# Kernel optimization log

Hardware: AMD Instinct MI355X
Metric: run time of the kernel (lower is better)

## Reference

```python
import jax, jax.numpy as jnp
import numpy as np

N_HASHES = 4
CHUNK = 144
REDUCTION = 4

# PyTorch bicubic (a=-0.75), align_corners=False, integer scale 2 ->
# fixed fractional offsets t=0.75 (even outputs) and t=0.25 (odd outputs).
_EW = jnp.array([-0.03515625, 0.26171875, 0.87890625, -0.10546875], jnp.float32)
_OW = _EW[::-1]


def _up2_axis(x, axis):
    n = x.shape[axis]
    pad = [(0, 0)] * x.ndim
    pad[axis] = (2, 2)
    xp = jnp.pad(x, pad, mode='edge')  # torch clamps border indices
    sl = lambda s: jax.lax.slice_in_dim(xp, s, s + n, axis=axis)
    even = sum(_EW[k] * sl(k) for k in range(4))
    odd = sum(_OW[k] * sl(k + 1) for k in range(4))
    out = jnp.stack([even, odd], axis=axis + 1)
    shp = list(x.shape)
    shp[axis] = 2 * n
    return out.reshape(shp)


def bicubic_up2(x):
    return _up2_axis(_up2_axis(x, 2), 3)


def conv2d(x, w, b, pad):
    y = jax.lax.conv_general_dilated(x, w, (1, 1), [(pad, pad), (pad, pad)],
                                     dimension_numbers=('NCHW', 'OIHW', 'NCHW'))
    return y + b[None, :, None, None]


def _adj(t):
    # attend to own + two adjacent buckets along chunk axis (axis=2)
    return jnp.concatenate([t, jnp.roll(t, 1, axis=2), jnp.roll(t, -1, axis=2)], axis=3)


def nlsa(x, wm, bm, wa, ba, rot):
    N, Cc, H, W = x.shape
    L = H * W
    xe = conv2d(x, wm, bm, 1).reshape(N, -1, L).transpose(0, 2, 1)  # [N,L,C]
    ye = conv2d(x, wa, ba, 0).reshape(N, -1, L).transpose(0, 2, 1)  # [N,L,C*red]
    C = xe.shape[-1]
    hash_buckets = min(L // CHUNK + (L // CHUNK) % 2, 128)
    # LSH: random rotations -> argmax bucket codes (non-differentiable, detached)
    rotated = jnp.einsum('btf,fhi->bhti', xe, rot)  # [N,h,L,hb//2]
    rotated = jnp.concatenate([rotated, -rotated], axis=-1)  # [N,h,L,hb]
    codes = jnp.argmax(rotated, axis=-1)  # [N,h,L]
    codes = codes + (jnp.arange(N_HASHES) * hash_buckets)[None, :, None]
    codes = jax.lax.stop_gradient(codes.reshape(N, -1))  # [N,h*L]
    indices = jnp.argsort(codes, axis=-1)
    undo = jnp.argsort(indices, axis=-1)
    mod = indices % L
    xs = jnp.take_along_axis(xe, mod[..., None], axis=1)  # [N,h*L,C]
    ys = jnp.take_along_axis(ye, mod[..., None], axis=1)  # [N,h*L,C*red]
    padding = (-L) % CHUNK
    xb = xs.reshape(N, N_HASHES, L, C)
    yb = ys.reshape(N, N_HASHES, L, C * REDUCTION)
    if padding:
        xb = jnp.concatenate([xb, xb[:, :, -padding:, :]], axis=2)
        yb = jnp.concatenate([yb, yb[:, :, -padding:, :]], axis=2)
    nch = xb.shape[2] // CHUNK
    xb = xb.reshape(N, N_HASHES, nch, CHUNK, C)
    yb = yb.reshape(N, N_HASHES, nch, CHUNK, C * REDUCTION)
    xm = xb / jnp.maximum(jnp.linalg.norm(xb, axis=-1, keepdims=True), 5e-5)
    xm = _adj(xm)      # [N,h,k,3*chunk,C]
    ybj = _adj(yb)     # [N,h,k,3*chunk,C*red]
    raw = jnp.einsum('bhkie,bhkje->bhkij', xb, xm)  # [N,h,k,chunk,3*chunk]
    bscore = jax.scipy.special.logsumexp(raw, axis=-1, keepdims=True)
    score = jnp.exp(raw - bscore)
    ret = jnp.einsum('bhkij,bhkje->bhkie', score, ybj)
    ret = ret.reshape(N, N_HASHES, -1, C * REDUCTION)
    bscore = bscore.reshape(N, N_HASHES, -1)
    if padding:
        ret = ret[:, :, :-padding]
        bscore = bscore[:, :, :-padding]
    ret = ret.reshape(N, -1, C * REDUCTION)
    bscore = bscore.reshape(N, -1)
    ret = jnp.take_along_axis(ret, undo[..., None], axis=1)
    bscore = jnp.take_along_axis(bscore, undo, axis=1)
    ret = ret.reshape(N, N_HASHES, L, C * REDUCTION)
    probs = jax.nn.softmax(bscore.reshape(N, N_HASHES, L, 1), axis=1)
    ret = jnp.sum(ret * probs, axis=1)  # [N,L,C*red]
    return ret.transpose(0, 2, 1).reshape(N, -1, H, W) + x


def setup_inputs() -> dict:
    key = jax.random.key(0)
    ks = jax.random.split(key, 8)
    w = lambda k, shape, fan: (jax.random.normal(k, shape, jnp.float32) / np.sqrt(fan)).astype(jnp.float32)
    return {
        'x': jax.random.normal(ks[0], (2, 64, 96, 96), jnp.float32),
        'w1': w(ks[1], (64, 64, 3, 3), 64 * 9), 'b1': jnp.zeros((64,), jnp.float32),
        'w2': w(ks[2], (64, 64, 3, 3), 64 * 9), 'b2': jnp.zeros((64,), jnp.float32),
        'wm': w(ks[3], (16, 64, 3, 3), 64 * 9), 'bm': jnp.zeros((16,), jnp.float32),
        'wa': w(ks[4], (64, 64, 1, 1), 64), 'ba': jnp.zeros((64,), jnp.float32),
        'rot': jax.random.normal(ks[5], (16, N_HASHES, 64), jnp.float32),  # [C, h, hash_buckets//2]
    }


def reference(x, w1, b1, w2, b2, wm, bm, wa, ba, rot):
    x = bicubic_up2(x)
    x = jax.nn.relu(conv2d(x, w1, b1, 1))
    x = jax.nn.relu(conv2d(x, w2, b2, 1))
    return nlsa(x, wm, bm, wa, ba, rot)
```

## Files before the change

### kernel.cpp

```cpp
#include <hip/hip_runtime.h>
#include <math.h>

#define NB 2
#define CIN 64
#define H0 96
#define W0 96
#define HH 192
#define WW 192
#define LL (HH*WW)
#define NHASH 4
#define CHK 144
#define NCHK 256
#define CE 16
#define CV 64
#define NBUCK 128
#define SEGL 576
#define NSEG 64

#define K_ROWB   80
#define V_ROWB   912
#define AT_KOFF  0
#define AT_VOFF  34560
#define AT_POFF  92928
#define AT_IOFF  104448
#define AT_LDS   106176

typedef __attribute__((ext_vector_type(8))) short short8_t;
typedef __attribute__((ext_vector_type(4))) float f32x4;
union FragU { unsigned int u[4]; int4 i; short8_t s; };

__device__ __forceinline__ unsigned int cvtpk_bf16(float a, float b){
  unsigned int r;
  asm("v_cvt_pk_bf16_f32 %0, %1, %2" : "=v"(r) : "v"(a), "v"(b));
  return r;
}
__device__ __forceinline__ float bfl(unsigned int u){ return __uint_as_float(u << 16); }
__device__ __forceinline__ float bfh(unsigned int u){ return __uint_as_float(u & 0xffff0000u); }

__global__ __launch_bounds__(256) void k_upsample(const float* __restrict__ x,
                                                  float* __restrict__ out){
  int idx = blockIdx.x*256 + threadIdx.x;
  if (idx >= NB*CIN*HH*WW) return;
  int ox = idx % WW; int t2 = idx / WW;
  int oy = t2 % HH;  t2 /= HH;
  int i = oy >> 1, a = oy & 1;
  int j = ox >> 1, b = ox & 1;
  const float e0=-0.03515625f, e1=0.26171875f, e2=0.87890625f, e3=-0.10546875f;
  float wy[4], wx[4]; int ty[4], tx[4];
  if (a){ wy[0]=e3; wy[1]=e2; wy[2]=e1; wy[3]=e0; } else { wy[0]=e0; wy[1]=e1; wy[2]=e2; wy[3]=e3; }
  if (b){ wx[0]=e3; wx[1]=e2; wx[2]=e1; wx[3]=e0; } else { wx[0]=e0; wx[1]=e1; wx[2]=e2; wx[3]=e3; }
  int offy = a ? -1 : -2, offx = b ? -1 : -2;
  #pragma unroll
  for (int k=0;k<4;k++){
    int t = i + offy + k; ty[k] = t<0?0:(t>H0-1?H0-1:t);
    int s = j + offx + k; tx[k] = s<0?0:(s>W0-1?W0-1:s);
  }
  const float* xp = x + (size_t)t2*H0*W0;
  float s = 0.f;
  #pragma unroll
  for (int ky=0;ky<4;ky++){
    const float* row = xp + ty[ky]*W0;
    float rs = 0.f;
    rs = fmaf(wx[0], row[tx[0]], rs);
    rs = fmaf(wx[1], row[tx[1]], rs);
    rs = fmaf(wx[2], row[tx[2]], rs);
    rs = fmaf(wx[3], row[tx[3]], rs);
    s = fmaf(wy[ky], rs, s);
  }
  out[idx] = s;
}

__global__ __launch_bounds__(256) void k_prepw(const float* __restrict__ w,
    unsigned short* __restrict__ wsT, int CO){
  int idx = blockIdx.x*256 + threadIdx.x;
  if (idx >= CO*64*9) return;
  int tap = idx % 9; int rem = idx / 9;
  int ci = rem % 64; int co = rem / 64;
  float v = w[(size_t)(co*64 + ci)*9 + tap];
  unsigned int hu = cvtpk_bf16(v, v) & 0xffffu;
  float hf = bfl(hu);
  unsigned int lu = cvtpk_bf16(v - hf, 0.f) & 0xffffu;
  int half = ci >> 5, kg = (ci >> 3) & 3, e = ci & 7;
  size_t base = ((size_t)(tap*2 + half)*2)*CO*32 + ((size_t)co*4 + kg)*8 + e;
  wsT[base]         = (unsigned short)hu;
  wsT[base + (size_t)CO*32] = (unsigned short)lu;
}

template<int CO, bool RELU, bool OUT_NLC>
__global__ __launch_bounds__(256) void k_conv3m(const float* __restrict__ in,
    const unsigned short* __restrict__ wsT, const float* __restrict__ bias,
    float* __restrict__ out){
  __shared__ unsigned short inH[3][66][64];
  __shared__ unsigned short inL[3][66][64];
  const int t = threadIdx.x;
  const int bx = blockIdx.x, y = blockIdx.y, n = blockIdx.z;
  const int x0 = bx*64;
  const int l = t & 63, w = t >> 6;
  const int lq = l & 15, kg = l >> 4;

  for (int e = t; e < 3072; e += 256){
    const int chunk = e & 15;
    const int strip = e >> 4;
    const int ci = strip & 63, row = strip >> 6;
    const int gy = y + row - 1;
    float4 v = make_float4(0.f,0.f,0.f,0.f);
    if (gy >= 0 && gy < HH)
      v = *(const float4*)&in[(((size_t)n*CIN + ci)*HH + gy)*WW + x0 + chunk*4];
    float vv[4] = {v.x, v.y, v.z, v.w};
    #pragma unroll
    for (int j = 0; j < 4; ++j){
      const int col = 1 + chunk*4 + j;
      const int sci = (((ci >> 3) ^ (col & 7)) << 3) | (ci & 7);
      unsigned int hu = cvtpk_bf16(vv[j], vv[j]);
      unsigned int lu = cvtpk_bf16(vv[j] - bfl(hu), 0.f);
      inH[row][col][sci] = (unsigned short)hu;
      inL[row][col][sci] = (unsigned short)lu;
    }
  }
  if (t < 192){
    const int ci = t & 63, row = t >> 6;
    const int gy = y + row - 1;
    const bool okY = (gy >= 0 && gy < HH);
    const float* ip = &in[(((size_t)n*CIN + ci)*HH + (size_t)(okY?gy:0))*WW];
    float vL = (okY && x0 >= 1) ? ip[x0-1] : 0.f;
    float vR = (okY && x0+64 < WW) ? ip[x0+64] : 0.f;
    unsigned int hL = cvtpk_bf16(vL, vL);
    unsigned int lLu = cvtpk_bf16(vL - bfl(hL), 0.f);
    unsigned int hR = cvtpk_bf16(vR, vR);
    unsigned int lRu = cvtpk_bf16(vR - bfl(hR), 0.f);
    const int sci0 = ci;
    const int sci65 = (((ci >> 3) ^ 1) << 3) | (ci & 7);
    inH[row][0][sci0]  = (unsigned short)hL;  inL[row][0][sci0]  = (unsigned short)lLu;
    inH[row][65][sci65] = (unsigned short)hR; inL[row][65][sci65] = (unsigned short)lRu;
  }
  __syncthreads();

  constexpr int NCT = CO/16;
  f32x4 acc[NCT];
  #pragma unroll
  for (int c=0;c<NCT;c++) acc[c] = (f32x4){0.f,0.f,0.f,0.f};
  const unsigned short* wlane = wsT + (size_t)lq*32 + (size_t)kg*8;

  #pragma unroll
  for (int tap=0; tap<9; ++tap){
    const int ky = tap/3, kx = tap - ky*3;
    const int col = w*16 + lq + kx;
    #pragma unroll
    for (int half=0; half<2; ++half){
      const int sci = ((((half<<2) | kg) ^ (col & 7)) << 3);
      FragU Bh, Bl;
      Bh.i = *(const int4*)&inH[ky][col][sci];
      Bl.i = *(const int4*)&inL[ky][col][sci];
      const unsigned short* wth = wlane + (size_t)((tap*2+half)*2)*CO*32;
      #pragma unroll
      for (int ct=0; ct<NCT; ++ct){
        FragU Ah, Al;
        Ah.i = *(const int4*)(wth + ct*512);
        Al.i = *(const int4*)(wth + CO*32 + ct*512);
        acc[ct] = __builtin_amdgcn_mfma_f32_16x16x32_bf16(Ah.s, Bl.s, acc[ct], 0,0,0);
        acc[ct] = __builtin_amdgcn_mfma_f32_16x16x32_bf16(Al.s, Bh.s, acc[ct], 0,0,0);
        acc[ct] = __builtin_amdgcn_mfma_f32_16x16x32_bf16(Ah.s, Bh.s, acc[ct], 0,0,0);
      }
    }
  }

  const int px = x0 + w*16 + lq;
  if constexpr (!OUT_NLC){
    #pragma unroll
    for (int ct=0; ct<NCT; ++ct){
      #pragma unroll
      for (int r=0; r<4; ++r){
        const int co = ct*16 + kg*4 + r;
        float v = acc[ct][r] + bias[co];
        if (RELU) v = fmaxf(v, 0.f);
        out[(((size_t)n*CO + co)*HH + y)*WW + px] = v;
      }
    }
  } else {
    #pragma unroll
    for (int r=0; r<4; ++r){
      const int co = kg*4 + r;
      float v = acc[0][r] + bias[co];
      if (RELU) v = fmaxf(v, 0.f);
      out[((size_t)n*LL + y*WW + px)*CO + co] = v;
    }
  }
}

__global__ __launch_bounds__(256) void k_conv1x1(const float* __restrict__ x2,
    const float* __restrict__ wa, const float* __restrict__ ba,
    float* __restrict__ ye){
  __shared__ float xs[64][64];
  __shared__ float wts[64][64];
  const int t = threadIdx.x;
  const int n = blockIdx.y;
  const int l0 = blockIdx.x*64;
  for (int e=t; e<4096; e+=256){
    int ci = e >> 6, l = e & 63;
    xs[ci][l]  = x2[((size_t)n*CIN+ci)*LL + l0 + l];
    wts[ci][l] = wa[(size_t)l*64 + ci];
  }
  __syncthreads();
  const int l = t & 63, cq = t >> 6;
  float acc[16];
  #pragma unroll
  for (int i=0;i<16;i++) acc[i] = ba[cq*16+i];
  for (int ci=0; ci<64; ci++){
    float xv = xs[ci][l];
    #pragma unroll
    for (int i=0;i<16;i++) acc[i] = fmaf(xv, wts[ci][cq*16+i], acc[i]);
  }
  float* op = &ye[((size_t)n*LL + l0 + l)*64 + cq*16];
  #pragma unroll
  for (int i=0;i<16;i++) op[i] = acc[i];
}

__global__ __launch_bounds__(128) void k_codes(const float* __restrict__ xe,
    const float* __restrict__ rot, unsigned char* __restrict__ codes){
  __shared__ float rs[NHASH][64][16];
  const int t = threadIdx.x;
  for (int e=t; e<4096; e+=128){
    int f = e >> 8; int rem = e & 255;
    int h = rem >> 6; int i = rem & 63;
    rs[h][i][f] = rot[((size_t)f*NHASH + h)*64 + i];
  }
  __syncthreads();
  const int n = blockIdx.y;
  const int l = blockIdx.x*128 + t;
  float q[16];
  const float* xr = &xe[((size_t)n*LL + l)*16];
  #pragma unroll
  for (int f=0;f<16;f++) q[f] = xr[f];
  #pragma unroll
  for (int h=0;h<NHASH;h++){
    float bp = -3.0e38f, bn = -3.0e38f; int ap=0, an=0;
    for (int i=0;i<64;i++){
      float s = 0.f;
      #pragma unroll
      for (int f=0;f<16;f++) s = fmaf(q[f], rs[h][i][f], s);
      if (s > bp){ bp = s; ap = i; }
      if (-s > bn){ bn = -s; an = i; }
    }
    int code = (bp >= bn) ? ap : (64 + an);
    codes[((size_t)n*NHASH + h)*LL + l] = (unsigned char)code;
  }
}

__global__ __launch_bounds__(256) void k_hist(const unsigned char* __restrict__ codes,
    unsigned int* __restrict__ segHist){
  __shared__ unsigned int h[NBUCK];
  const int t = threadIdx.x;
  if (t < NBUCK) h[t] = 0;
  __syncthreads();
  const int n = blockIdx.z, hh = blockIdx.y, s = blockIdx.x;
  const unsigned char* cp = codes + ((size_t)n*NHASH + hh)*LL + (size_t)s*SEGL;
  for (int e=t; e<SEGL; e+=256) atomicAdd(&h[cp[e]], 1u);
  __syncthreads();
  if (t < NBUCK)
    segHist[(((size_t)(n*NHASH+hh))*NSEG + s)*NBUCK + t] = h[t];
}

__global__ __launch_bounds__(128) void k_scan(unsigned int* __restrict__ segHist){
  __shared__ unsigned int tot[NBUCK];
  __shared__ unsigned int base[NBUCK];
  const int b = threadIdx.x;
  const size_t off = (size_t)blockIdx.x * NSEG * NBUCK;
  unsigned int run = 0;
  for (int s=0;s<NSEG;s++){
    unsigned int v = segHist[off + (size_t)s*NBUCK + b];
    segHist[off + (size_t)s*NBUCK + b] = run;
    run += v;
  }
  tot[b] = run;
  __syncthreads();
  if (b==0){ unsigned int r=0; for (int i=0;i<NBUCK;i++){ base[i]=r; r+=tot[i]; } }
  __syncthreads();
  const unsigned int bb = base[b];
  for (int s=0;s<NSEG;s++) segHist[off + (size_t)s*NBUCK + b] += bb;
}

__global__ __launch_bounds__(256) void k_rank(const unsigned char* __restrict__ codes,
    const unsigned int* __restrict__ segHist, int* __restrict__ sortPos,
    int* __restrict__ srtIdx){
  __shared__ unsigned int cw[SEGL/4];
  __shared__ unsigned int sbase[NBUCK];
  const int t = threadIdx.x;
  const int n = blockIdx.z, hh = blockIdx.y, s = blockIdx.x;
  const size_t cb = ((size_t)n*NHASH + hh)*LL + (size_t)s*SEGL;
  const unsigned int* cp32 = (const unsigned int*)(codes + cb);
  for (int e=t; e<SEGL/4; e+=256) cw[e] = cp32[e];
  if (t < NBUCK)
    sbase[t] = segHist[(((size_t)(n*NHASH+hh))*NSEG + s)*NBUCK + t];
  __syncthreads();
  const size_t ob = ((size_t)n*NHASH + hh)*LL;
  for (int e=t; e<SEGL; e+=256){
    unsigned int c = (cw[e>>2] >> ((e&3)*8)) & 0xffu;
    unsigned int mul = c * 0x01010101u;
    int cnt = 0;
    const int nw = e >> 2;
    for (int wi=0; wi<nw; wi++){
      unsigned int v = cw[wi] ^ mul;
      unsigned int t1 = (v & 0x7f7f7f7fu) + 0x7f7f7f7fu;
      unsigned int z = ~(t1 | v) & 0x80808080u;
      cnt += __popc(z);
    }
    unsigned int lastw = cw[nw];
    const int nbp = e & 3;
    for (int bp=0; bp<nbp; bp++)
      if (((lastw >> (bp*8)) & 0xffu) == c) cnt++;
    int pos = (int)sbase[c] + cnt;
    int l = s*SEGL + e;
    sortPos[ob + l] = pos;
    srtIdx[ob + pos] = l;
  }
}

__global__ __launch_bounds__(576) void k_attn(const float* __restrict__ xe,
    const float* __restrict__ ye, const int* __restrict__ srtIdx,
    unsigned short* __restrict__ retS, float* __restrict__ bscore){
  extern __shared__ char smem[];
  unsigned short* Kq = (unsigned short*)(smem + AT_KOFF);
  char* Vt  = smem + AT_VOFF;
  char* Pst = smem + AT_POFF;
  int* lkI  = (int*)(smem + AT_IOFF);

  const int t = threadIdx.x;
  const int k = blockIdx.x, hh = blockIdx.y, n = blockIdx.z;
  const size_t sb = ((size_t)n*NHASH + hh)*LL;
  const int l = t & 63, w = t >> 6;
  const int lq16 = l & 15, g = l >> 4;

  if (t < 432){
    const int c3 = t / CHK, jl = t - c3*CHK;
    const int kc = (c3==0) ? k : ((c3==1) ? ((k+NCHK-1)&(NCHK-1)) : ((k+1)&(NCHK-1)));
    const int lk = srtIdx[sb + (size_t)kc*CHK + jl];
    lkI[t] = lk;
    const float4* xr = (const float4*)&xe[((size_t)n*LL + lk)*16];
    float4 v0 = xr[0], v1 = xr[1], v2 = xr[2], v3 = xr[3];
    float f[16] = {v0.x,v0.y,v0.z,v0.w, v1.x,v1.y,v1.z,v1.w,
                   v2.x,v2.y,v2.z,v2.w, v3.x,v3.y,v3.z,v3.w};
    float ss = 0.f;
    #pragma unroll
    for (int i=0;i<16;i++) ss = fmaf(f[i], f[i], ss);
    const float inv = 1.f / fmaxf(sqrtf(ss), 5e-5f);
    #pragma unroll
    for (int i=0;i<16;i++) f[i] *= inv;
    unsigned int kh[8], klo[8];
    #pragma unroll
    for (int i=0;i<8;i++) kh[i] = cvtpk_bf16(f[2*i], f[2*i+1]);
    #pragma unroll
    for (int i=0;i<8;i++)
      klo[i] = cvtpk_bf16(f[2*i] - bfl(kh[i]), f[2*i+1] - bfh(kh[i]));
    int4* kr = (int4*)((char*)Kq + t*K_ROWB);
    kr[0] = make_int4((int)kh[0],(int)kh[1],(int)kh[2],(int)kh[3]);
    kr[1] = make_int4((int)kh[4],(int)kh[5],(int)kh[6],(int)kh[7]);
    kr[2] = make_int4((int)klo[0],(int)klo[1],(int)klo[2],(int)klo[3]);
    kr[3] = make_int4((int)klo[4],(int)klo[5],(int)klo[6],(int)klo[7]);
  }
  if (t < 512){
    int c = t >> 3, jp = t & 7;
    *(unsigned int*)(Vt + c*V_ROWB + 864 + jp*4) = 0u;
  }
  __syncthreads();

  #pragma unroll 4
  for (int it=0; it<24; ++it){
    const int e = t + it*576;
    const int jp = e >> 6, c = e & 63;
    const float a = ye[((size_t)n*LL + lkI[2*jp  ])*64 + c];
    const float b = ye[((size_t)n*LL + lkI[2*jp+1])*64 + c];
    *(unsigned int*)(Vt + c*V_ROWB + jp*4) = cvtpk_bf16(a, b);
  }
  const int qg = w*16 + lq16;
  const int pq = k*CHK + qg;
  FragU b1, b2;
  {
    const int lq = lkI[qg];
    const float4* qp = (const float4*)&xe[((size_t)n*LL + lq)*16 + (size_t)(g&1)*8];
    float4 qa = qp[0], qb = qp[1];
    b1.u[0] = cvtpk_bf16(qa.x, qa.y); b1.u[1] = cvtpk_bf16(qa.z, qa.w);
    b1.u[2] = cvtpk_bf16(qb.x, qb.y); b1.u[3] = cvtpk_bf16(qb.z, qb.w);
    if (g < 2){
      b2.u[0] = cvtpk_bf16(qa.x - bfl(b1.u[0]), qa.y - bfh(b1.u[0]));
      b2.u[1] = cvtpk_bf16(qa.z - bfl(b1.u[1]), qa.w - bfh(b1.u[1]));
      b2.u[2] = cvtpk_bf16(qb.x - bfl(b1.u[2]), qb.y - bfh(b1.u[2]));
      b2.u[3] = cvtpk_bf16(qb.z - bfl(b1.u[3]), qb.w - bfh(b1.u[3]));
    } else {
      b2.u[0]=0u; b2.u[1]=0u; b2.u[2]=0u; b2.u[3]=0u;
    }
  }
  __syncthreads();

  const char* Kb = (const char*)Kq + lq16*K_ROWB + g*16;
  float m = -3.0e38f;
  for (int t27=0; t27<27; ++t27){
    FragU a; a.i = *(const int4*)(Kb + (size_t)t27*16*K_ROWB);
    f32x4 C = {0.f,0.f,0.f,0.f};
    C = __builtin_amdgcn_mfma_f32_16x16x32_bf16(a.s, b2.s, C, 0, 0, 0);
    C = __builtin_amdgcn_mfma_f32_16x16x32_bf16(a.s, b1.s, C, 0, 0, 0);
    m = fmaxf(m, fmaxf(fmaxf(C[0],C[1]), fmaxf(C[2],C[3])));
  }
  m = fmaxf(m, __shfl_xor(m, 16));
  m = fmaxf(m, __shfl_xor(m, 32));

  float sum = 0.f;
  f32x4 O0 = {0.f,0.f,0.f,0.f}, O1 = O0, O2 = O0, O3 = O0;
  char* Pw = Pst + w*1280;
  for (int u=0; u<14; ++u){
    #pragma unroll
    for (int sub=0; sub<2; ++sub){
      const int t27 = u*2 + sub;
      uint2 pw;
      if (t27 < 27){
        FragU a; a.i = *(const int4*)(Kb + (size_t)t27*16*K_ROWB);
        f32x4 C = {0.f,0.f,0.f,0.f};
        C = __builtin_amdgcn_mfma_f32_16x16x32_bf16(a.s, b2.s, C, 0, 0, 0);
        C = __builtin_amdgcn_mfma_f32_16x16x32_bf16(a.s, b1.s, C, 0, 0, 0);
        const float p0 = __expf(C[0]-m), p1 = __expf(C[1]-m);
        const float p2 = __expf(C[2]-m), p3 = __expf(C[3]-m);
        sum += (p0+p1) + (p2+p3);
        pw = make_uint2(cvtpk_bf16(p0,p1), cvtpk_bf16(p2,p3));
      } else {
        pw = make_uint2(0u, 0u);
      }
      *(uint2*)(Pw + lq16*K_ROWB + sub*32 + g*8) = pw;
    }
    asm volatile("s_waitcnt lgkmcnt(0)" ::: "memory");
    __builtin_amdgcn_sched_barrier(0);
    FragU bp; bp.i = *(const int4*)(Pw + lq16*K_ROWB + g*16);
    const char* Vb = Vt + lq16*V_ROWB + u*64 + g*16;
    FragU av;
    av.i = *(const int4*)(Vb);             O0 = __builtin_amdgcn_mfma_f32_16x16x32_bf16(av.s, bp.s, O0, 0,0,0);
    av.i = *(const int4*)(Vb + 16*V_ROWB); O1 = __builtin_amdgcn_mfma_f32_16x16x32_bf16(av.s, bp.s, O1, 0,0,0);
    av.i = *(const int4*)(Vb + 32*V_ROWB); O2 = __builtin_amdgcn_mfma_f32_16x16x32_bf16(av.s, bp.s, O2, 0,0,0);
    av.i = *(const int4*)(Vb + 48*V_ROWB); O3 = __builtin_amdgcn_mfma_f32_16x16x32_bf16(av.s, bp.s, O3, 0,0,0);
  }
  sum += __shfl_xor(sum, 16);
  sum += __shfl_xor(sum, 32);
  const float linv = 1.f / sum;

  unsigned short* op = &retS[(sb + pq)*64];
  {
    uint2 s0 = make_uint2(cvtpk_bf16(O0[0]*linv, O0[1]*linv), cvtpk_bf16(O0[2]*linv, O0[3]*linv));
    uint2 s1 = make_uint2(cvtpk_bf16(O1[0]*linv, O1[1]*linv), cvtpk_bf16(O1[2]*linv, O1[3]*linv));
    uint2 s2 = make_uint2(cvtpk_bf16(O2[0]*linv, O2[1]*linv), cvtpk_bf16(O2[2]*linv, O2[3]*linv));
    uint2 s3 = make_uint2(cvtpk_bf16(O3[0]*linv, O3[1]*linv), cvtpk_bf16(O3[2]*linv, O3[3]*linv));
    *(uint2*)(op +  0 + g*4) = s0;
    *(uint2*)(op + 16 + g*4) = s1;
    *(uint2*)(op + 32 + g*4) = s2;
    *(uint2*)(op + 48 + g*4) = s3;
  }
  if (g == 0) bscore[sb + pq] = m + logf(sum);
}

__global__ __launch_bounds__(256) void k_combine(const unsigned short* __restrict__ retS,
    const float* __restrict__ bscore, const int* __restrict__ sortPos,
    const float* __restrict__ x2, float* __restrict__ out){
  const int idx = blockIdx.x*256 + threadIdx.x;
  if (idx >= NB*LL) return;
  const int l = idx % LL, n = idx / LL;
  float bs[NHASH]; int pp[NHASH];
  #pragma unroll
  for (int h=0;h<NHASH;h++){
    size_t sb = ((size_t)n*NHASH + h)*LL;
    int p = sortPos[sb + l];
    pp[h] = p; bs[h] = bscore[sb + p];
  }
  float m = fmaxf(fmaxf(bs[0],bs[1]), fmaxf(bs[2],bs[3]));
  float wsum = 0.f; float wv[NHASH];
  #pragma unroll
  for (int h=0;h<NHASH;h++){ wv[h] = expf(bs[h]-m); wsum += wv[h]; }
  const float winv = 1.f / wsum;
  float o[64];
  #pragma unroll
  for (int i=0;i<64;i++) o[i]=0.f;
  #pragma unroll
  for (int h=0;h<NHASH;h++){
    const float wh = wv[h]*winv;
    const uint4* rp = (const uint4*)&retS[(((size_t)n*NHASH + h)*LL + pp[h])*64];
    #pragma unroll
    for (int i2=0;i2<8;i2++){
      uint4 v = rp[i2];
      o[i2*8+0] = fmaf(wh, bfl(v.x), o[i2*8+0]);
      o[i2*8+1] = fmaf(wh, bfh(v.x), o[i2*8+1]);
      o[i2*8+2] = fmaf(wh, bfl(v.y), o[i2*8+2]);
      o[i2*8+3] = fmaf(wh, bfh(v.y), o[i2*8+3]);
      o[i2*8+4] = fmaf(wh, bfl(v.z), o[i2*8+4]);
      o[i2*8+5] = fmaf(wh, bfh(v.z), o[i2*8+5]);
      o[i2*8+6] = fmaf(wh, bfl(v.w), o[i2*8+6]);
      o[i2*8+7] = fmaf(wh, bfh(v.w), o[i2*8+7]);
    }
  }
  #pragma unroll
  for (int c=0;c<64;c++){
    size_t oi = ((size_t)n*64 + c)*LL + l;
    out[oi] = o[c] + x2[oi];
  }
}

extern "C" void kernel_launch(void* const* d_in, const int* in_sizes, int n_in,
                              void* d_out, int out_size, void* d_ws, size_t ws_size,
                              hipStream_t stream){
  const float* x   = (const float*)d_in[0];
  const float* w1  = (const float*)d_in[1];
  const float* b1  = (const float*)d_in[2];
  const float* w2  = (const float*)d_in[3];
  const float* b2  = (const float*)d_in[4];
  const float* wm  = (const float*)d_in[5];
  const float* bm  = (const float*)d_in[6];
  const float* wa  = (const float*)d_in[7];
  const float* ba  = (const float*)d_in[8];
  const float* rot = (const float*)d_in[9];
  float* outp = (float*)d_out;
  char* ws = (char*)d_ws;
  const size_t FM = (size_t)NB*CIN*HH*WW*sizeof(float);
  float* x0u = (float*)(ws + 0);
  float* y1  = (float*)(ws + FM);
  float* x2  = (float*)(ws + 2*FM);
  float* xe  = (float*)(ws + 3*FM);
  float* ye  = (float*)(ws + 3*FM + (size_t)NB*LL*CE*sizeof(float));
  char* p = ws + 3*FM + (size_t)NB*LL*CE*sizeof(float) + FM;
  unsigned char* codes = (unsigned char*)p; p += (size_t)NB*NHASH*LL;
  unsigned int* segHist = (unsigned int*)p; p += (size_t)NB*NHASH*NSEG*NBUCK*sizeof(unsigned int);
  int* sortPos = (int*)p; p += (size_t)NB*NHASH*LL*sizeof(int);
  int* srtIdx  = (int*)p; p += (size_t)NB*NHASH*LL*sizeof(int);
  float* bscore = (float*)p; p += (size_t)NB*NHASH*LL*sizeof(float);
  unsigned short* wsT1 = (unsigned short*)p; p += (size_t)9*2*2*64*32*sizeof(unsigned short);
  unsigned short* wsT2 = (unsigned short*)p; p += (size_t)9*2*2*64*32*sizeof(unsigned short);
  unsigned short* wsTm = (unsigned short*)p; p += (size_t)9*2*2*16*32*sizeof(unsigned short);
  unsigned short* retS = (unsigned short*)ws;
  if (ws_size < (size_t)(p - ws)) return;

  hipFuncSetAttribute((const void*)k_attn,
                      hipFuncAttributeMaxDynamicSharedMemorySize, AT_LDS);

  k_prepw<<<dim3((64*64*9+255)/256), dim3(256), 0, stream>>>(w1, wsT1, 64);
  k_prepw<<<dim3((64*64*9+255)/256), dim3(256), 0, stream>>>(w2, wsT2, 64);
  k_prepw<<<dim3((16*64*9+255)/256), dim3(256), 0, stream>>>(wm, wsTm, 16);
  k_upsample<<<dim3((NB*CIN*HH*WW+255)/256), dim3(256), 0, stream>>>(x, x0u);
  k_conv3m<64,true,false><<<dim3(3, HH, NB), dim3(256), 0, stream>>>(x0u, wsT1, b1, y1);
  k_conv3m<64,true,false><<<dim3(3, HH, NB), dim3(256), 0, stream>>>(y1, wsT2, b2, x2);
  k_conv3m<16,false,true><<<dim3(3, HH, NB), dim3(256), 0, stream>>>(x2, wsTm, bm, xe);
  k_conv1x1<<<dim3(LL/64, NB), dim3(256), 0, stream>>>(x2, wa, ba, ye);
  k_codes<<<dim3(LL/128, NB), dim3(128), 0, stream>>>(xe, rot, codes);
  k_hist<<<dim3(NSEG, NHASH, NB), dim3(256), 0, stream>>>(codes, segHist);
  k_scan<<<dim3(NB*NHASH), dim3(128), 0, stream>>>(segHist);
  k_rank<<<dim3(NSEG, NHASH, NB), dim3(256), 0, stream>>>(codes, segHist, sortPos, srtIdx);
  k_attn<<<dim3(NCHK, NHASH, NB), dim3(576), AT_LDS, stream>>>(xe, ye, srtIdx, retS, bscore);
  k_combine<<<dim3((NB*LL+255)/256), dim3(256), 0, stream>>>(retS, bscore, sortPos, x2, outp);
}
```

Before: 411.8 us.

## Drop max pass in LSH attention via Cauchy-Schwarz bound, bf16 values, pre-gathered keys

The first pass that found each query's row maximum is removed. Because keys are unit-normalised, the query norm bounds every score, so it serves as the softmax shift and the score matrix is computed only once. The 1x1 value conv now writes bf16 directly, which halves the gather traffic in attention. Keys are optionally pre-normalised and sorted into a global buffer by a separate kernel, letting attention skip the per-block key LDS staging and use less LDS. The workspace layout is reorganised so these buffers fit, with a fallback path when the workspace is smaller. The fixed shift may underflow exp for queries whose best score is far below the norm bound.

```diff
diff --git a/kernel.cpp b/kernel.cpp
--- a/kernel.cpp
+++ b/kernel.cpp
@@ -19,11 +19,14 @@
 
 #define K_ROWB   80
 #define V_ROWB   912
-#define AT_KOFF  0
-#define AT_VOFF  34560
-#define AT_POFF  92928
-#define AT_IOFF  104448
-#define AT_LDS   106176
+#define P_ROWB   72
+#define KQ_SZB   34560
+#define VT_SZB   58368
+#define PST_SZB  10368
+#define LKI_SZB  1728
+#define QN_SZB   576
+#define LDS_T1   (VT_SZB + PST_SZB + LKI_SZB)
+#define LDS_T2   (KQ_SZB + VT_SZB + PST_SZB + LKI_SZB + QN_SZB)
 
 typedef __attribute__((ext_vector_type(8))) short short8_t;
 typedef __attribute__((ext_vector_type(4))) float f32x4;
@@ -189,7 +192,7 @@
 
 __global__ __launch_bounds__(256) void k_conv1x1(const float* __restrict__ x2,
     const float* __restrict__ wa, const float* __restrict__ ba,
-    float* __restrict__ ye){
+    unsigned short* __restrict__ yeB){
   __shared__ float xs[64][64];
   __shared__ float wts[64][64];
   const int t = threadIdx.x;
@@ -210,9 +213,12 @@
     #pragma unroll
     for (int i=0;i<16;i++) acc[i] = fmaf(xv, wts[ci][cq*16+i], acc[i]);
   }
-  float* op = &ye[((size_t)n*LL + l0 + l)*64 + cq*16];
-  #pragma unroll
-  for (int i=0;i<16;i++) op[i] = acc[i];
+  unsigned int wds[8];
+  #pragma unroll
+  for (int i=0;i<8;i++) wds[i] = cvtpk_bf16(acc[2*i], acc[2*i+1]);
+  uint4* op = (uint4*)&yeB[((size_t)n*LL + l0 + l)*64 + cq*16];
+  op[0] = make_uint4(wds[0],wds[1],wds[2],wds[3]);
+  op[1] = make_uint4(wds[4],wds[5],wds[6],wds[7]);
 }
 
 __global__ __launch_bounds__(128) void k_codes(const float* __restrict__ xe,
@@ -315,14 +321,50 @@
   }
 }
 
-__global__ __launch_bounds__(576) void k_attn(const float* __restrict__ xe,
-    const float* __restrict__ ye, const int* __restrict__ srtIdx,
+__global__ __launch_bounds__(256) void k_gatherK(const float* __restrict__ xe,
+    const int* __restrict__ srtIdx, unsigned short* __restrict__ Ksrt,
+    float* __restrict__ normQ){
+  const int idx = blockIdx.x*256 + threadIdx.x;
+  if (idx >= NB*NHASH*LL) return;
+  const int n = idx / (NHASH*LL);
+  const int lk = srtIdx[idx];
+  const float4* xr = (const float4*)&xe[((size_t)n*LL + lk)*16];
+  float4 v0 = xr[0], v1 = xr[1], v2 = xr[2], v3 = xr[3];
+  float f[16] = {v0.x,v0.y,v0.z,v0.w, v1.x,v1.y,v1.z,v1.w,
+                 v2.x,v2.y,v2.z,v2.w, v3.x,v3.y,v3.z,v3.w};
+  float ss = 0.f;
+  #pragma unroll
+  for (int i=0;i<16;i++) ss = fmaf(f[i], f[i], ss);
+  const float nq = sqrtf(ss);
+  normQ[idx] = nq;
+  const float inv = 1.f / fmaxf(nq, 5e-5f);
+  #pragma unroll
+  for (int i=0;i<16;i++) f[i] *= inv;
+  unsigned int kh[8], klo[8];
+  #pragma unroll
+  for (int i=0;i<8;i++) kh[i] = cvtpk_bf16(f[2*i], f[2*i+1]);
+  #pragma unroll
+  for (int i=0;i<8;i++)
+    klo[i] = cvtpk_bf16(f[2*i] - bfl(kh[i]), f[2*i+1] - bfh(kh[i]));
+  int4* kr = (int4*)(Ksrt + (size_t)idx*32);
+  kr[0] = make_int4((int)kh[0],(int)kh[1],(int)kh[2],(int)kh[3]);
+  kr[1] = make_int4((int)kh[4],(int)kh[5],(int)kh[6],(int)kh[7]);
+  kr[2] = make_int4((int)klo[0],(int)klo[1],(int)klo[2],(int)klo[3]);
+  kr[3] = make_int4((int)klo[4],(int)klo[5],(int)klo[6],(int)klo[7]);
+}
+
+template<int TIER>
+__global__ __launch_bounds__(576) void k_attn2(const float* __restrict__ xe,
+    const unsigned short* __restrict__ yeB, const int* __restrict__ srtIdx,
+    const unsigned short* __restrict__ Ksrt, const float* __restrict__ normQ,
     unsigned short* __restrict__ retS, float* __restrict__ bscore){
   extern __shared__ char smem[];
-  unsigned short* Kq = (unsigned short*)(smem + AT_KOFF);
-  char* Vt  = smem + AT_VOFF;
-  char* Pst = smem + AT_POFF;
-  int* lkI  = (int*)(smem + AT_IOFF);
+  constexpr int KQOFF = (TIER==2) ? KQ_SZB : 0;
+  unsigned short* Kq = (unsigned short*)smem;
+  char* Vt  = smem + KQOFF;
+  char* Pst = Vt + VT_SZB;
+  int* lkI  = (int*)(Pst + PST_SZB);
+  float* qn = (float*)(Pst + PST_SZB + LKI_SZB);
 
   const int t = threadIdx.x;
   const int k = blockIdx.x, hh = blockIdx.y, n = blockIdx.z;
@@ -335,27 +377,31 @@
     const int kc = (c3==0) ? k : ((c3==1) ? ((k+NCHK-1)&(NCHK-1)) : ((k+1)&(NCHK-1)));
     const int lk = srtIdx[sb + (size_t)kc*CHK + jl];
     lkI[t] = lk;
-    const float4* xr = (const float4*)&xe[((size_t)n*LL + lk)*16];
-    float4 v0 = xr[0], v1 = xr[1], v2 = xr[2], v3 = xr[3];
-    float f[16] = {v0.x,v0.y,v0.z,v0.w, v1.x,v1.y,v1.z,v1.w,
-                   v2.x,v2.y,v2.z,v2.w, v3.x,v3.y,v3.z,v3.w};
-    float ss = 0.f;
-    #pragma unroll
-    for (int i=0;i<16;i++) ss = fmaf(f[i], f[i], ss);
-    const float inv = 1.f / fmaxf(sqrtf(ss), 5e-5f);
-    #pragma unroll
-    for (int i=0;i<16;i++) f[i] *= inv;
-    unsigned int kh[8], klo[8];
-    #pragma unroll
-    for (int i=0;i<8;i++) kh[i] = cvtpk_bf16(f[2*i], f[2*i+1]);
-    #pragma unroll
-    for (int i=0;i<8;i++)
-      klo[i] = cvtpk_bf16(f[2*i] - bfl(kh[i]), f[2*i+1] - bfh(kh[i]));
-    int4* kr = (int4*)((char*)Kq + t*K_ROWB);
-    kr[0] = make_int4((int)kh[0],(int)kh[1],(int)kh[2],(int)kh[3]);
-    kr[1] = make_int4((int)kh[4],(int)kh[5],(int)kh[6],(int)kh[7]);
-    kr[2] = make_int4((int)klo[0],(int)klo[1],(int)klo[2],(int)klo[3]);
-    kr[3] = make_int4((int)klo[4],(int)klo[5],(int)klo[6],(int)klo[7]);
+    if constexpr (TIER==2){
+      const float4* xr = (const float4*)&xe[((size_t)n*LL + lk)*16];
+      float4 v0 = xr[0], v1 = xr[1], v2 = xr[2], v3 = xr[3];
+      float f[16] = {v0.x,v0.y,v0.z,v0.w, v1.x,v1.y,v1.z,v1.w,
+                     v2.x,v2.y,v2.z,v2.w, v3.x,v3.y,v3.z,v3.w};
+      float ss = 0.f;
+      #pragma unroll
+      for (int i=0;i<16;i++) ss = fmaf(f[i], f[i], ss);
+      const float nq = sqrtf(ss);
+      if (c3 == 0) qn[jl] = nq;
+      const float inv = 1.f / fmaxf(nq, 5e-5f);
+      #pragma unroll
+      for (int i=0;i<16;i++) f[i] *= inv;
+      unsigned int kh[8], klo[8];
+      #pragma unroll
+      for (int i=0;i<8;i++) kh[i] = cvtpk_bf16(f[2*i], f[2*i+1]);
+      #pragma unroll
+      for (int i=0;i<8;i++)
+        klo[i] = cvtpk_bf16(f[2*i] - bfl(kh[i]), f[2*i+1] - bfh(kh[i]));
+      int4* kr = (int4*)((char*)Kq + t*K_ROWB);
+      kr[0] = make_int4((int)kh[0],(int)kh[1],(int)kh[2],(int)kh[3]);
+      kr[1] = make_int4((int)kh[4],(int)kh[5],(int)kh[6],(int)kh[7]);
+      kr[2] = make_int4((int)klo[0],(int)klo[1],(int)klo[2],(int)klo[3]);
+      kr[3] = make_int4((int)klo[4],(int)klo[5],(int)klo[6],(int)klo[7]);
+    }
   }
   if (t < 512){
     int c = t >> 3, jp = t & 7;
@@ -367,67 +413,65 @@
   for (int it=0; it<24; ++it){
     const int e = t + it*576;
     const int jp = e >> 6, c = e & 63;
-    const float a = ye[((size_t)n*LL + lkI[2*jp  ])*64 + c];
-    const float b = ye[((size_t)n*LL + lkI[2*jp+1])*64 + c];
-    *(unsigned int*)(Vt + c*V_ROWB + jp*4) = cvtpk_bf16(a, b);
+    const unsigned int a = yeB[((size_t)n*LL + lkI[2*jp  ])*64 + c];
+    const unsigned int b = yeB[((size_t)n*LL + lkI[2*jp+1])*64 + c];
+    *(unsigned int*)(Vt + c*V_ROWB + jp*4) = a | (b << 16);
   }
   const int qg = w*16 + lq16;
   const int pq = k*CHK + qg;
   FragU b1, b2;
-  {
-    const int lq = lkI[qg];
-    const float4* qp = (const float4*)&xe[((size_t)n*LL + lq)*16 + (size_t)(g&1)*8];
-    float4 qa = qp[0], qb = qp[1];
-    b1.u[0] = cvtpk_bf16(qa.x, qa.y); b1.u[1] = cvtpk_bf16(qa.z, qa.w);
-    b1.u[2] = cvtpk_bf16(qb.x, qb.y); b1.u[3] = cvtpk_bf16(qb.z, qb.w);
-    if (g < 2){
-      b2.u[0] = cvtpk_bf16(qa.x - bfl(b1.u[0]), qa.y - bfh(b1.u[0]));
-      b2.u[1] = cvtpk_bf16(qa.z - bfl(b1.u[1]), qa.w - bfh(b1.u[1]));
-      b2.u[2] = cvtpk_bf16(qb.x - bfl(b1.u[2]), qb.y - bfh(b1.u[2]));
-      b2.u[3] = cvtpk_bf16(qb.z - bfl(b1.u[3]), qb.w - bfh(b1.u[3]));
-    } else {
-      b2.u[0]=0u; b2.u[1]=0u; b2.u[2]=0u; b2.u[3]=0u;
-    }
-  }
-  __syncthreads();
-
-  const char* Kb = (const char*)Kq + lq16*K_ROWB + g*16;
-  float m = -3.0e38f;
-  for (int t27=0; t27<27; ++t27){
-    FragU a; a.i = *(const int4*)(Kb + (size_t)t27*16*K_ROWB);
-    f32x4 C = {0.f,0.f,0.f,0.f};
-    C = __builtin_amdgcn_mfma_f32_16x16x32_bf16(a.s, b2.s, C, 0, 0, 0);
-    C = __builtin_amdgcn_mfma_f32_16x16x32_bf16(a.s, b1.s, C, 0, 0, 0);
-    m = fmaxf(m, fmaxf(fmaxf(C[0],C[1]), fmaxf(C[2],C[3])));
-  }
-  m = fmaxf(m, __shfl_xor(m, 16));
-  m = fmaxf(m, __shfl_xor(m, 32));
+  float nq_;
+  if constexpr (TIER==1){
+    const unsigned short* qrow = Ksrt + (sb + pq)*32;
+    b1.i = *(const int4*)(qrow + (g&1)*8);
+    if (g < 2) b2.i = *(const int4*)(qrow + 16 + (g&1)*8);
+    else { b2.u[0]=0u; b2.u[1]=0u; b2.u[2]=0u; b2.u[3]=0u; }
+    nq_ = normQ[sb + pq];
+  } else {
+    const char* qrow = (const char*)Kq + qg*K_ROWB;
+    b1.i = *(const int4*)(qrow + (g&1)*16);
+    if (g < 2) b2.i = *(const int4*)(qrow + 32 + (g&1)*16);
+    else { b2.u[0]=0u; b2.u[1]=0u; b2.u[2]=0u; b2.u[3]=0u; }
+    nq_ = qn[qg];
+  }
+  const float msc = fmaxf(nq_, 5e-5f);
+  __syncthreads();
 
   float sum = 0.f;
   f32x4 O0 = {0.f,0.f,0.f,0.f}, O1 = O0, O2 = O0, O3 = O0;
-  char* Pw = Pst + w*1280;
+  char* Pw = Pst + w*(16*P_ROWB);
   for (int u=0; u<14; ++u){
     #pragma unroll
     for (int sub=0; sub<2; ++sub){
       const int t27 = u*2 + sub;
       uint2 pw;
       if (t27 < 27){
-        FragU a; a.i = *(const int4*)(Kb + (size_t)t27*16*K_ROWB);
+        FragU a;
+        if constexpr (TIER==1){
+          const int c3 = t27 / 9;
+          const int kc = (c3==0) ? k : ((c3==1) ? ((k+NCHK-1)&(NCHK-1)) : ((k+1)&(NCHK-1)));
+          const int row16 = (t27 - c3*9)*16;
+          a.i = *(const int4*)(Ksrt + (sb + (size_t)kc*CHK + row16 + lq16)*32 + g*8);
+        } else {
+          a.i = *(const int4*)((const char*)Kq + (size_t)(t27*16 + lq16)*K_ROWB + g*16);
+        }
         f32x4 C = {0.f,0.f,0.f,0.f};
         C = __builtin_amdgcn_mfma_f32_16x16x32_bf16(a.s, b2.s, C, 0, 0, 0);
         C = __builtin_amdgcn_mfma_f32_16x16x32_bf16(a.s, b1.s, C, 0, 0, 0);
-        const float p0 = __expf(C[0]-m), p1 = __expf(C[1]-m);
-        const float p2 = __expf(C[2]-m), p3 = __expf(C[3]-m);
+        const float p0 = __expf(fmaf(msc, C[0], -nq_));
+        const float p1 = __expf(fmaf(msc, C[1], -nq_));
+        const float p2 = __expf(fmaf(msc, C[2], -nq_));
+        const float p3 = __expf(fmaf(msc, C[3], -nq_));
         sum += (p0+p1) + (p2+p3);
         pw = make_uint2(cvtpk_bf16(p0,p1), cvtpk_bf16(p2,p3));
       } else {
         pw = make_uint2(0u, 0u);
       }
-      *(uint2*)(Pw + lq16*K_ROWB + sub*32 + g*8) = pw;
+      *(uint2*)(Pw + lq16*P_ROWB + sub*32 + g*8) = pw;
     }
     asm volatile("s_waitcnt lgkmcnt(0)" ::: "memory");
     __builtin_amdgcn_sched_barrier(0);
-    FragU bp; bp.i = *(const int4*)(Pw + lq16*K_ROWB + g*16);
+    FragU bp; bp.i = *(const int4*)(Pw + lq16*P_ROWB + g*16);
     const char* Vb = Vt + lq16*V_ROWB + u*64 + g*16;
     FragU av;
     av.i = *(const int4*)(Vb);             O0 = __builtin_amdgcn_mfma_f32_16x16x32_bf16(av.s, bp.s, O0, 0,0,0);
@@ -450,7 +494,7 @@
     *(uint2*)(op + 32 + g*4) = s2;
     *(uint2*)(op + 48 + g*4) = s3;
   }
-  if (g == 0) bscore[sb + pq] = m + logf(sum);
+  if (g == 0) bscore[sb + pq] = nq_ + logf(sum);
 }
 
 __global__ __launch_bounds__(256) void k_combine(const unsigned short* __restrict__ retS,
@@ -513,26 +557,39 @@
   const float* rot = (const float*)d_in[9];
   float* outp = (float*)d_out;
   char* ws = (char*)d_ws;
-  const size_t FM = (size_t)NB*CIN*HH*WW*sizeof(float);
-  float* x0u = (float*)(ws + 0);
-  float* y1  = (float*)(ws + FM);
-  float* x2  = (float*)(ws + 2*FM);
-  float* xe  = (float*)(ws + 3*FM);
-  float* ye  = (float*)(ws + 3*FM + (size_t)NB*LL*CE*sizeof(float));
-  char* p = ws + 3*FM + (size_t)NB*LL*CE*sizeof(float) + FM;
-  unsigned char* codes = (unsigned char*)p; p += (size_t)NB*NHASH*LL;
-  unsigned int* segHist = (unsigned int*)p; p += (size_t)NB*NHASH*NSEG*NBUCK*sizeof(unsigned int);
-  int* sortPos = (int*)p; p += (size_t)NB*NHASH*LL*sizeof(int);
-  int* srtIdx  = (int*)p; p += (size_t)NB*NHASH*LL*sizeof(int);
-  float* bscore = (float*)p; p += (size_t)NB*NHASH*LL*sizeof(float);
-  unsigned short* wsT1 = (unsigned short*)p; p += (size_t)9*2*2*64*32*sizeof(unsigned short);
-  unsigned short* wsT2 = (unsigned short*)p; p += (size_t)9*2*2*64*32*sizeof(unsigned short);
-  unsigned short* wsTm = (unsigned short*)p; p += (size_t)9*2*2*16*32*sizeof(unsigned short);
-  unsigned short* retS = (unsigned short*)ws;
-  if (ws_size < (size_t)(p - ws)) return;
-
-  hipFuncSetAttribute((const void*)k_attn,
-                      hipFuncAttributeMaxDynamicSharedMemorySize, AT_LDS);
+  const size_t FM   = (size_t)NB*CIN*HH*WW*sizeof(float);
+  const size_t YEB  = (size_t)NB*LL*64*2;
+  const size_t RETB = (size_t)NB*NHASH*LL*64*2;
+  const size_t NHL4 = (size_t)NB*NHASH*LL*4;
+
+  char* p = ws;
+  unsigned short* yeB = (unsigned short*)p;  p += YEB;
+  char* regA = p;                            p += RETB;
+  float* x2  = (float*)p;                    p += FM;
+  float* xe  = (float*)p;                    p += (size_t)NB*LL*CE*sizeof(float);
+  unsigned char* codes = (unsigned char*)p;  p += (size_t)NB*NHASH*LL;
+  unsigned int* segHist = (unsigned int*)p;  p += (size_t)NB*NHASH*NSEG*NBUCK*4;
+  int* sortPos = (int*)p;                    p += NHL4;
+  int* srtIdx  = (int*)p;                    p += NHL4;
+  float* bscore = (float*)p;                 p += NHL4;
+  unsigned short* wsT1 = (unsigned short*)p; p += (size_t)9*2*2*64*32*2;
+  unsigned short* wsT2 = (unsigned short*)p; p += (size_t)9*2*2*64*32*2;
+  unsigned short* wsTm = (unsigned short*)p; p += (size_t)9*2*2*16*32*2;
+  const size_t needT2 = (size_t)(p - ws);
+  unsigned short* Ksrt = (unsigned short*)p; p += (size_t)NB*NHASH*LL*32*2;
+  float* normQ = (float*)p;                  p += NHL4;
+  const size_t needT1 = (size_t)(p - ws);
+
+  unsigned short* retS = (unsigned short*)regA;
+  float* x0u = (float*)regA;
+  float* y1  = (float*)(regA + FM);
+  if (ws_size < needT2) return;
+  const bool preg = (ws_size >= needT1);
+
+  hipFuncSetAttribute((const void*)k_attn2<1>,
+                      hipFuncAttributeMaxDynamicSharedMemorySize, LDS_T1);
+  hipFuncSetAttribute((const void*)k_attn2<2>,
+                      hipFuncAttributeMaxDynamicSharedMemorySize, LDS_T2);
 
   k_prepw<<<dim3((64*64*9+255)/256), dim3(256), 0, stream>>>(w1, wsT1, 64);
   k_prepw<<<dim3((64*64*9+255)/256), dim3(256), 0, stream>>>(w2, wsT2, 64);
@@ -541,11 +598,18 @@
   k_conv3m<64,true,false><<<dim3(3, HH, NB), dim3(256), 0, stream>>>(x0u, wsT1, b1, y1);
   k_conv3m<64,true,false><<<dim3(3, HH, NB), dim3(256), 0, stream>>>(y1, wsT2, b2, x2);
   k_conv3m<16,false,true><<<dim3(3, HH, NB), dim3(256), 0, stream>>>(x2, wsTm, bm, xe);
-  k_conv1x1<<<dim3(LL/64, NB), dim3(256), 0, stream>>>(x2, wa, ba, ye);
+  k_conv1x1<<<dim3(LL/64, NB), dim3(256), 0, stream>>>(x2, wa, ba, yeB);
   k_codes<<<dim3(LL/128, NB), dim3(128), 0, stream>>>(xe, rot, codes);
   k_hist<<<dim3(NSEG, NHASH, NB), dim3(256), 0, stream>>>(codes, segHist);
   k_scan<<<dim3(NB*NHASH), dim3(128), 0, stream>>>(segHist);
   k_rank<<<dim3(NSEG, NHASH, NB), dim3(256), 0, stream>>>(codes, segHist, sortPos, srtIdx);
-  k_attn<<<dim3(NCHK, NHASH, NB), dim3(576), AT_LDS, stream>>>(xe, ye, srtIdx, retS, bscore);
+  if (preg){
+    k_gatherK<<<dim3((NB*NHASH*LL+255)/256), dim3(256), 0, stream>>>(xe, srtIdx, Ksrt, normQ);
+    k_attn2<1><<<dim3(NCHK, NHASH, NB), dim3(576), LDS_T1, stream>>>(
+        xe, yeB, srtIdx, Ksrt, normQ, retS, bscore);
+  } else {
+    k_attn2<2><<<dim3(NCHK, NHASH, NB), dim3(576), LDS_T2, stream>>>(
+        xe, yeB, srtIdx, Ksrt, normQ, retS, bscore);
+  }
   k_combine<<<dim3((NB*LL+255)/256), dim3(256), 0, stream>>>(retS, bscore, sortPos, x2, outp);
 }
```

Measured after the change: 352.3 us. -14.4%, faster.
